# Kernel tuning notes

Hardware: AMD Instinct MI355X
Metric: run time of the kernel (lower is better)

The kernel has to match this reference:

```python
import jax, jax.numpy as jnp
import numpy as np

B, S, H, NH, HD, P, MAXP = 2, 2048, 2048, 16, 128, 2048, 4096
EPS = 1e-06


def setup_inputs() -> dict:
    key = jax.random.key(0)
    ks = jax.random.split(key, 8)
    sc = lambda fan: 1.0 / np.sqrt(fan)
    hidden_states = jax.random.normal(ks[0], (B, S, H), jnp.float32)
    # rotary table: freqs[p] = p * inv_freq, duplicated (non-interleaved) -> [MAXP,1,1,HD]
    inv_freq = 1.0 / (500000.0 ** (np.arange(0, HD, 2, dtype=np.float32) / HD))
    ang = np.outer(np.arange(MAXP, dtype=np.float32), inv_freq)  # [MAXP, HD/2]
    freqs = jnp.asarray(np.concatenate([ang, ang], axis=-1).reshape(MAXP, 1, 1, HD), jnp.float32)
    positions = jnp.tile(jnp.arange(S, dtype=jnp.int32), B)  # [T] = [B*S]
    Wqk = jax.random.normal(ks[1], (2 * P, H), jnp.float32) * sc(H)
    Wv = jax.random.normal(ks[2], (P, H), jnp.float32) * sc(H)
    Wo = jax.random.normal(ks[3], (H, P), jnp.float32) * sc(P)
    conv1_w = jax.random.normal(ks[4], (H // 2, H, 2, 1), jnp.float32) * sc(2 * H)
    conv1_b = jax.random.normal(ks[5], (H // 2,), jnp.float32) * 0.01
    conv2_w = jax.random.normal(ks[6], (H, H // 2, 2, 1), jnp.float32) * sc(H)
    conv2_b = jax.random.normal(ks[7], (H,), jnp.float32) * 0.01
    ln_w = jnp.ones((H,), jnp.float32)
    lf1_cache = jnp.zeros((B, H, 1, 1), jnp.float32)
    lf2_cache = jnp.zeros((B, H // 2, 1, 1), jnp.float32)
    return dict(hidden_states=hidden_states, freqs=freqs, positions=positions,
                Wqk=Wqk, Wv=Wv, Wo=Wo, conv1_w=conv1_w, conv1_b=conv1_b,
                conv2_w=conv2_w, conv2_b=conv2_b, ln_w=ln_w,
                lf1_cache=lf1_cache, lf2_cache=lf2_cache)


def _rmsnorm(x, w, eps=EPS):
    return x * w * jax.lax.rsqrt(jnp.mean(x * x, axis=-1, keepdims=True) + eps)


def _rotate_half(x):
    x1, x2 = jnp.split(x, 2, axis=-1)
    return jnp.concatenate([-x2, x1], axis=-1)


def _forward(hidden_states, freqs, positions, Wqk, Wv, Wo,
             conv1_w, conv1_b, conv2_w, conv2_b, ln_w, lf1_cache, lf2_cache):
    # v projection on raw hidden states
    v = jnp.einsum('bsh,ph->bsp', hidden_states, Wv)  # [B,S,P]

    # --- LocalizedFiltering (causal (2,1) convs with 1-step caches) ---
    x = hidden_states                                     # [B,S,H]
    xc = jnp.concatenate([lf1_cache[:, :, 0, 0][:, None, :], x], axis=1)  # [B,S+1,H]
    w1a, w1b = conv1_w[:, :, 0, 0], conv1_w[:, :, 1, 0]   # [H/2,H]
    y1 = (jnp.einsum('bsh,oh->bso', xc[:, :-1], w1a)
          + jnp.einsum('bsh,oh->bso', xc[:, 1:], w1b) + conv1_b)  # [B,S,H/2]
    y1c = jnp.concatenate([lf2_cache[:, :, 0, 0][:, None, :], y1], axis=1)  # [B,S+1,H/2]
    w2a, w2b = conv2_w[:, :, 0, 0], conv2_w[:, :, 1, 0]   # [H,H/2]
    y2 = (jnp.einsum('bso,ho->bsh', y1c[:, :-1], w2a)
          + jnp.einsum('bso,ho->bsh', y1c[:, 1:], w2b) + conv2_b)  # [B,S,H]
    lf_out = _rmsnorm(y2 + x, ln_w)                       # [B,S,H]
    lf1_new = xc[:, -1][:, :, None, None]                 # [B,H,1,1]
    lf2_new = y1c[:, -1][:, :, None, None]                # [B,H/2,1,1]

    # --- QK projection + RoPE ---
    qk = jnp.einsum('bsh,ph->bsp', lf_out, Wqk).reshape(B, S, NH, 2 * HD)
    q, k = jnp.split(qk, 2, axis=-1)                      # [B,S,NH,HD] each
    f = freqs[positions].reshape(B, S, 1, HD)             # per-token angles
    cos_, sin_ = jnp.cos(f), jnp.sin(f)
    q = q * cos_ + _rotate_half(q) * sin_
    k = k * cos_ + _rotate_half(k) * sin_

    # --- causal SDPA ---
    scale = HD ** -0.5
    vh = v.reshape(B, S, NH, HD)
    scores = jnp.einsum('bqhd,bkhd->bhqk', q, k) * scale  # [B,NH,S,S]
    mask = jnp.tril(jnp.ones((S, S), bool))
    scores = jnp.where(mask, scores, jnp.float32(-1e30))
    probs = jax.nn.softmax(scores, axis=-1)
    attn = jnp.einsum('bhqk,bkhd->bqhd', probs, vh).reshape(B * S, P)

    output = attn @ Wo.T                                  # [T,H]
    return output, lf1_new, lf2_new


def reference(hidden_states, freqs, positions, Wqk, Wv, Wo,
              conv1_w, conv1_b, conv2_w, conv2_b, ln_w, lf1_cache, lf2_cache):
    return _forward(hidden_states, freqs, positions, Wqk, Wv, Wo,
                    conv1_w, conv1_b, conv2_w, conv2_b, ln_w, lf1_cache, lf2_cache)
```

## Files before the change

### kernel.cpp

```cpp
#include <hip/hip_runtime.h>
#include <hip/hip_bf16.h>
#include <stdint.h>

#define Bb 2
#define Ss 2048
#define Hh 2048
#define NHh 16
#define HDd 128
#define Pp 2048
#define Mm 4096

typedef __bf16 bf16x8 __attribute__((ext_vector_type(8)));
typedef float f32x4 __attribute__((ext_vector_type(4)));
typedef float f32x16 __attribute__((ext_vector_type(16)));
typedef __hip_bfloat16 bf16_t;

static __device__ __forceinline__ bf16_t f2b(float f) { return __float2bfloat16(f); }
static __device__ __forceinline__ float b2f(bf16_t b) { return __bfloat162float(b); }

__global__ void k_pack_weights(const float* __restrict__ Wv, const float* __restrict__ Wqk,
                               const float* __restrict__ Wo, const float* __restrict__ c1w,
                               const float* __restrict__ c2w, bf16_t* __restrict__ wv_bf,
                               bf16_t* __restrict__ wqk_bf, bf16_t* __restrict__ wo_bf,
                               bf16_t* __restrict__ w1cat, bf16_t* __restrict__ w2cat) {
  const int M4 = 4 * 1024 * 1024;
  int stride = gridDim.x * blockDim.x;
  for (int i = blockIdx.x * blockDim.x + threadIdx.x; i < 6 * M4; i += stride) {
    if (i < M4) {
      wv_bf[i] = f2b(Wv[i]);
    } else if (i < 3 * M4) {
      int j = i - M4;
      wqk_bf[j] = f2b(Wqk[j]);
    } else if (i < 4 * M4) {
      int j = i - 3 * M4;
      wo_bf[j] = f2b(Wo[j]);
    } else if (i < 5 * M4) {
      int j = i - 4 * M4;
      int o = j >> 12, hp = j & 4095;
      int t = hp >> 11, h = hp & 2047;
      w1cat[j] = f2b(c1w[((size_t)o * 2048 + h) * 2 + t]);
    } else {
      int j = i - 5 * M4;
      int o = j >> 11, cp = j & 2047;
      int t = cp >> 10, c = cp & 1023;
      w2cat[j] = f2b(c2w[((size_t)o * 1024 + c) * 2 + t]);
    }
  }
}

__global__ void k_pack_x(const float* __restrict__ x, const float* __restrict__ lf1,
                         bf16_t* __restrict__ xcat) {
  int stride = gridDim.x * blockDim.x;
  for (int i = blockIdx.x * blockDim.x + threadIdx.x; i < Mm * Hh; i += stride) {
    int m = i >> 11, h = i & 2047;
    int b = m >> 11, s = m & 2047;
    float xv = x[i];
    xcat[(size_t)m * 4096 + 2048 + h] = f2b(xv);
    float xs = (s == 0) ? lf1[b * 2048 + h] : x[i - 2048];
    xcat[(size_t)m * 4096 + h] = f2b(xs);
  }
}

__global__ void k_lf2fill(const float* __restrict__ lf2, bf16_t* __restrict__ y1cat) {
  int i = blockIdx.x * 256 + threadIdx.x;
  if (i >= 2048) return;
  int b = i >> 10, c = i & 1023;
  y1cat[(size_t)(b * 2048) * 2048 + c] = f2b(lf2[b * 1024 + c]);
}

__global__ __launch_bounds__(256) void k_rmsnorm(const float* __restrict__ y2,
                                                 const float* __restrict__ x,
                                                 const float* __restrict__ w,
                                                 bf16_t* __restrict__ out) {
  int m = blockIdx.x;
  const float* yr = y2 + (size_t)m * 2048;
  const float* xr = x + (size_t)m * 2048;
  int tid = threadIdx.x;
  float t[8];
  float ss = 0.0f;
#pragma unroll
  for (int j = 0; j < 8; ++j) {
    int idx = tid + j * 256;
    float v = yr[idx] + xr[idx];
    t[j] = v;
    ss += v * v;
  }
#pragma unroll
  for (int o = 32; o >= 1; o >>= 1) ss += __shfl_xor(ss, o, 64);
  __shared__ float red[4];
  if ((tid & 63) == 0) red[tid >> 6] = ss;
  __syncthreads();
  float tot = red[0] + red[1] + red[2] + red[3];
  float rs = rsqrtf(tot * (1.0f / 2048.0f) + 1e-6f);
#pragma unroll
  for (int j = 0; j < 8; ++j) {
    int idx = tid + j * 256;
    out[(size_t)m * 2048 + idx] = f2b(t[j] * w[idx] * rs);
  }
}

__global__ void k_tails(const float* __restrict__ x, const bf16_t* __restrict__ y1cat,
                        float* __restrict__ out) {
  int i = blockIdx.x * 256 + threadIdx.x;
  if (i >= 4096 + 2048) return;
  const size_t off = (size_t)Mm * Hh;
  if (i < 4096) {
    int b = i >> 11, h = i & 2047;
    out[off + i] = x[((size_t)b * 2048 + 2047) * 2048 + h];
  } else {
    int j = i - 4096;
    int b = j >> 10, c = j & 1023;
    out[off + 4096 + j] = b2f(y1cat[((size_t)b * 2048 + 2047) * 2048 + 1024 + c]);
  }
}

#define EPI_F32 0
#define EPI_Y1CAT 1
#define EPI_ROPE 2
#define EPI_VT 3

template <int EPI, int HAS_BIAS>
__global__ __launch_bounds__(256) void gemm_epi(const bf16_t* __restrict__ A,
                                                const bf16_t* __restrict__ Bw,
                                                void* __restrict__ C1, void* __restrict__ C2,
                                                const float* __restrict__ bias,
                                                const int* __restrict__ posp,
                                                const float* __restrict__ freqs,
                                                int M, int N, int K, int lda) {
  constexpr int SMEM_BYTES = (EPI == EPI_ROPE || EPI == EPI_VT) ? 34816 : 32768;
  __shared__ __align__(16) char smem[SMEM_BYTES];
  bf16_t* lA = (bf16_t*)smem;
  bf16_t* lB = (bf16_t*)(smem + 16384);

  const int tid = threadIdx.x;
  const int lane = tid & 63;
  const int row0 = blockIdx.x * 128;
  const int col0 = blockIdx.y * 128;
  const int wr = ((tid >> 6) >> 1) * 64;
  const int wc = ((tid >> 6) & 1) * 64;
  const int lr = lane & 15;
  const int lg = lane >> 4;

  f32x4 acc[4][4];
#pragma unroll
  for (int i = 0; i < 4; ++i)
#pragma unroll
    for (int j = 0; j < 4; ++j) acc[i][j] = f32x4{0.f, 0.f, 0.f, 0.f};

  for (int k0 = 0; k0 < K; k0 += 64) {
    __syncthreads();
#pragma unroll
    for (int is = 0; is < 4; ++is) {
      const int e = is * 2048 + tid * 8;
      const int r = e >> 6, c = e & 63;
      __builtin_amdgcn_global_load_lds(
          (const __attribute__((address_space(1))) void*)(A + (size_t)(row0 + r) * lda + (k0 + c)),
          (__attribute__((address_space(3))) void*)(&lA[e]), 16, 0, 0);
      __builtin_amdgcn_global_load_lds(
          (const __attribute__((address_space(1))) void*)(Bw + (size_t)(col0 + r) * K + (k0 + c)),
          (__attribute__((address_space(3))) void*)(&lB[e]), 16, 0, 0);
    }
    __syncthreads();
#pragma unroll
    for (int ks = 0; ks < 2; ++ks) {
      bf16x8 af[4], bfg[4];
#pragma unroll
      for (int mi = 0; mi < 4; ++mi)
        af[mi] = *reinterpret_cast<const bf16x8*>(&lA[(wr + mi * 16 + lr) * 64 + ks * 32 + lg * 8]);
#pragma unroll
      for (int ni = 0; ni < 4; ++ni)
        bfg[ni] = *reinterpret_cast<const bf16x8*>(&lB[(wc + ni * 16 + lr) * 64 + ks * 32 + lg * 8]);
#pragma unroll
      for (int mi = 0; mi < 4; ++mi)
#pragma unroll
        for (int ni = 0; ni < 4; ++ni)
          acc[mi][ni] = __builtin_amdgcn_mfma_f32_16x16x32_bf16(af[mi], bfg[ni], acc[mi][ni], 0, 0, 0);
    }
  }

  if constexpr (EPI == EPI_F32) {
#pragma unroll
    for (int mi = 0; mi < 4; ++mi)
#pragma unroll
      for (int ni = 0; ni < 4; ++ni) {
        const int cc = col0 + wc + ni * 16 + lr;
        float bv = HAS_BIAS ? bias[cc] : 0.0f;
#pragma unroll
        for (int r = 0; r < 4; ++r) {
          const int rr = row0 + wr + mi * 16 + lg * 4 + r;
          ((float*)C1)[(size_t)rr * N + cc] = acc[mi][ni][r] + bv;
        }
      }
  } else if constexpr (EPI == EPI_Y1CAT) {
    bf16_t* y1cat = (bf16_t*)C1;
#pragma unroll
    for (int mi = 0; mi < 4; ++mi)
#pragma unroll
      for (int ni = 0; ni < 4; ++ni) {
        const int cc = col0 + wc + ni * 16 + lr;
        float bv = HAS_BIAS ? bias[cc] : 0.0f;
#pragma unroll
        for (int r = 0; r < 4; ++r) {
          const int rr = row0 + wr + mi * 16 + lg * 4 + r;
          bf16_t v = f2b(acc[mi][ni][r] + bv);
          y1cat[(size_t)rr * 2048 + 1024 + cc] = v;
          if ((rr & 2047) != 2047) y1cat[(size_t)(rr + 1) * 2048 + cc] = v;
        }
      }
  } else if constexpr (EPI == EPI_ROPE) {
    __syncthreads();
    bf16_t(*tile)[136] = (bf16_t(*)[136])smem;
#pragma unroll
    for (int mi = 0; mi < 4; ++mi)
#pragma unroll
      for (int ni = 0; ni < 4; ++ni) {
        const int cl = wc + ni * 16 + lr;
#pragma unroll
        for (int r = 0; r < 4; ++r) {
          const int rl = wr + mi * 16 + lg * 4 + r;
          tile[rl][cl] = f2b(acc[mi][ni][r]);
        }
      }
    __syncthreads();
    const int r = tid >> 1, half = tid & 1;
    const int m = row0 + r;
    const int s = m & 2047, bb = m >> 11;
    const int cb = col0 >> 7, h = cb >> 1, isk = cb & 1;
    const int pos = posp[m];
    const float* fr = freqs + (size_t)pos * HDd;
    const float qs = isk ? 1.0f : 0.08838834764831845f;
    bf16_t* dst = (bf16_t*)(isk ? C2 : C1) + ((size_t)(bb * NHh + h) * Ss + s) * HDd + half * 64;
#pragma unroll
    for (int j = 0; j < 8; ++j) {
      bf16x8 lo = *reinterpret_cast<const bf16x8*>(&tile[r][j * 8]);
      bf16x8 hv = *reinterpret_cast<const bf16x8*>(&tile[r][64 + j * 8]);
      bf16x8 ov;
#pragma unroll
      for (int e = 0; e < 8; ++e) {
        float f = fr[j * 8 + e];
        float sn, cs;
        __sincosf(f, &sn, &cs);
        float v0 = b2f((bf16_t)lo[e]), v1 = b2f((bf16_t)hv[e]);
        float o = half ? (v1 * cs + v0 * sn) : (v0 * cs - v1 * sn);
        ov[e] = (__bf16)f2b(o * qs);
      }
      *reinterpret_cast<bf16x8*>(dst + j * 8) = ov;
    }
  } else if constexpr (EPI == EPI_VT) {
    __syncthreads();
    bf16_t(*ttile)[136] = (bf16_t(*)[136])smem;
#pragma unroll
    for (int mi = 0; mi < 4; ++mi)
#pragma unroll
      for (int ni = 0; ni < 4; ++ni) {
        const int cl = wc + ni * 16 + lr;
#pragma unroll
        for (int r = 0; r < 4; ++r) {
          const int rl = wr + mi * 16 + lg * 4 + r;
          ttile[cl][rl] = f2b(acc[mi][ni][r]);
        }
      }
    __syncthreads();
    const int d = tid >> 1, sc = tid & 1;
    const int bb = row0 >> 11, s0 = row0 & 2047, h = col0 >> 7;
    bf16_t* dst = (bf16_t*)C1 + ((size_t)(bb * NHh + h) * HDd + d) * Ss + s0 + sc * 64;
#pragma unroll
    for (int j = 0; j < 8; ++j)
      *reinterpret_cast<bf16x8*>(dst + j * 8) =
          *reinterpret_cast<const bf16x8*>(&ttile[d][sc * 64 + j * 8]);
  }
}

__global__ __launch_bounds__(256) void k_attn3(const bf16_t* __restrict__ qa,
                                               const bf16_t* __restrict__ ka,
                                               const bf16_t* __restrict__ vt,
                                               bf16_t* __restrict__ attn_out) {
  __shared__ bf16_t kbuf[64 * 128];
  __shared__ bf16_t vbuf[128 * 64];
  __shared__ bf16_t pbuf[4][32 * 64];

  const int tid = threadIdx.x;
  const int wave = tid >> 6, lane = tid & 63;
  const int l31 = lane & 31, hi = lane >> 5;
  const int bh = blockIdx.x;
  const int yy = blockIdx.y;
  const int jq = (yy < 8) ? (15 - yy) : (yy - 8);
  const int q0b = jq * 128;
  const int q0w = q0b + wave * 32;
  const int b = bh >> 4, h = bh & 15;

  const bf16_t* Q = qa + (size_t)bh * Ss * HDd;
  const bf16_t* K = ka + (size_t)bh * Ss * HDd;
  const bf16_t* V = vt + (size_t)bh * HDd * Ss;
  char* pw = (char*)&pbuf[wave][0];

  bf16x8 qf[8];
#pragma unroll
  for (int dc = 0; dc < 8; ++dc)
    qf[dc] = *reinterpret_cast<const bf16x8*>(&Q[(size_t)(q0w + l31) * HDd + dc * 16 + hi * 8]);

  f32x16 o[4];
#pragma unroll
  for (int db = 0; db < 4; ++db)
#pragma unroll
    for (int i = 0; i < 16; ++i) o[db][i] = 0.f;
  float mrun = -3e38f, lrun = 0.f;
  const int qrow = q0w + l31;

  const int nkt = q0b / 64 + 2;
  bf16x8 pk[4], pv[4];
  auto loadt = [&](int kt) {
    const int k0l = kt * 64;
#pragma unroll
    for (int i = 0; i < 4; ++i) {
      pk[i] = *reinterpret_cast<const bf16x8*>(
          &K[(size_t)(k0l + (tid >> 2)) * HDd + ((tid & 3) + 4 * i) * 8]);
      pv[i] = *reinterpret_cast<const bf16x8*>(
          &V[(size_t)(tid >> 1) * Ss + k0l + ((tid & 1) * 4 + i) * 8]);
    }
  };
  loadt(0);

  for (int kt = 0; kt < nkt; ++kt) {
    const int k0 = kt * 64;
    __syncthreads();
    {
      const int kr = tid >> 2, vr = tid >> 1;
#pragma unroll
      for (int i = 0; i < 4; ++i) {
        const int ku = (tid & 3) + 4 * i;
        *reinterpret_cast<bf16x8*>((char*)kbuf + kr * 256 + ((ku * 16) ^ ((kr & 7) << 4))) = pk[i];
        const int vu = (tid & 1) * 4 + i;
        *reinterpret_cast<bf16x8*>((char*)vbuf + vr * 128 + ((vu * 16) ^ ((vr & 7) << 4))) = pv[i];
      }
    }
    __syncthreads();
    if (kt + 1 < nkt) loadt(kt + 1);
    if (k0 > q0w + 31) continue;

    f32x16 s0, s1;
#pragma unroll
    for (int i = 0; i < 16; ++i) { s0[i] = 0.f; s1[i] = 0.f; }
    __builtin_amdgcn_s_setprio(1);
#pragma unroll
    for (int dc = 0; dc < 8; ++dc) {
      const int off = (dc * 32 + hi * 16) ^ ((l31 & 7) << 4);
      bf16x8 kf0 = *reinterpret_cast<const bf16x8*>((const char*)kbuf + l31 * 256 + off);
      bf16x8 kf1 = *reinterpret_cast<const bf16x8*>((const char*)kbuf + (32 + l31) * 256 + off);
      s0 = __builtin_amdgcn_mfma_f32_32x32x16_bf16(kf0, qf[dc], s0, 0, 0, 0);
      s1 = __builtin_amdgcn_mfma_f32_32x32x16_bf16(kf1, qf[dc], s1, 0, 0, 0);
    }
    __builtin_amdgcn_s_setprio(0);
    if (k0 + 63 > q0w) {
#pragma unroll
      for (int reg = 0; reg < 16; ++reg) {
        const int key = k0 + (reg & 3) + 8 * (reg >> 2) + 4 * hi;
        if (key > qrow) s0[reg] = -1e30f;
        if (key + 32 > qrow) s1[reg] = -1e30f;
      }
    }
    float pm = fmaxf(s0[0], s1[0]);
#pragma unroll
    for (int reg = 1; reg < 16; ++reg) pm = fmaxf(pm, fmaxf(s0[reg], s1[reg]));
    pm = fmaxf(pm, __shfl_xor(pm, 32, 64));
    if (!__all(pm - mrun <= 8.0f)) {
      const float mnew = fmaxf(mrun, pm);
      const float alpha = __expf(mrun - mnew);
      lrun *= alpha;
#pragma unroll
      for (int reg = 0; reg < 16; ++reg) {
        const int r = (reg & 3) + 8 * (reg >> 2) + 4 * hi;
        const float ar = __shfl(alpha, r, 64);
        o[0][reg] *= ar; o[1][reg] *= ar; o[2][reg] *= ar; o[3][reg] *= ar;
      }
      mrun = mnew;
    }
    float psum = 0.f;
#pragma unroll
    for (int reg = 0; reg < 16; ++reg) {
      s0[reg] = __expf(s0[reg] - mrun); psum += s0[reg];
      s1[reg] = __expf(s1[reg] - mrun); psum += s1[reg];
    }
    psum += __shfl_xor(psum, 32, 64);
    lrun += psum;
#pragma unroll
    for (int g = 0; g < 4; ++g) {
      uint32_t w0, w1, w2, w3;
      asm("v_cvt_pk_bf16_f32 %0, %1, %2" : "=v"(w0) : "v"(s0[4 * g]), "v"(s0[4 * g + 1]));
      asm("v_cvt_pk_bf16_f32 %0, %1, %2" : "=v"(w1) : "v"(s0[4 * g + 2]), "v"(s0[4 * g + 3]));
      asm("v_cvt_pk_bf16_f32 %0, %1, %2" : "=v"(w2) : "v"(s1[4 * g]), "v"(s1[4 * g + 1]));
      asm("v_cvt_pk_bf16_f32 %0, %1, %2" : "=v"(w3) : "v"(s1[4 * g + 2]), "v"(s1[4 * g + 3]));
      const int key0 = 8 * g + 4 * hi;
      const int sw = (l31 & 7) << 4;
      *reinterpret_cast<uint2*>(pw + l31 * 128 + ((key0 * 2) ^ sw)) = uint2{w0, w1};
      *reinterpret_cast<uint2*>(pw + l31 * 128 + (((key0 + 32) * 2) ^ sw)) = uint2{w2, w3};
    }
    __builtin_amdgcn_s_setprio(1);
#pragma unroll
    for (int kc = 0; kc < 4; ++kc) {
      bf16x8 pa = *reinterpret_cast<const bf16x8*>(
          pw + l31 * 128 + ((kc * 32 + hi * 16) ^ ((l31 & 7) << 4)));
#pragma unroll
      for (int db = 0; db < 4; ++db) {
        const int d = db * 32 + l31;
        bf16x8 vf = *reinterpret_cast<const bf16x8*>(
            (const char*)vbuf + d * 128 + ((kc * 32 + hi * 16) ^ ((d & 7) << 4)));
        o[db] = __builtin_amdgcn_mfma_f32_32x32x16_bf16(pa, vf, o[db], 0, 0, 0);
      }
    }
    __builtin_amdgcn_s_setprio(0);
  }
  const float linv = 1.0f / lrun;
#pragma unroll
  for (int reg = 0; reg < 16; ++reg) {
    const int r = (reg & 3) + 8 * (reg >> 2) + 4 * hi;
    const float li = __shfl(linv, r, 64);
    const int qr = q0w + r;
#pragma unroll
    for (int db = 0; db < 4; ++db) {
      attn_out[(size_t)(b * 2048 + qr) * 2048 + h * 128 + db * 32 + l31] = f2b(o[db][reg] * li);
    }
  }
}

extern "C" void kernel_launch(void* const* d_in, const int* in_sizes, int n_in,
                              void* d_out, int out_size, void* d_ws, size_t ws_size,
                              hipStream_t stream) {
  const float* x     = (const float*)d_in[0];
  const float* freqs = (const float*)d_in[1];
  const int*   pos   = (const int*)d_in[2];
  const float* Wqk   = (const float*)d_in[3];
  const float* Wv    = (const float*)d_in[4];
  const float* Wo    = (const float*)d_in[5];
  const float* c1w   = (const float*)d_in[6];
  const float* c1b   = (const float*)d_in[7];
  const float* c2w   = (const float*)d_in[8];
  const float* c2b   = (const float*)d_in[9];
  const float* lnw   = (const float*)d_in[10];
  const float* lf1   = (const float*)d_in[11];
  const float* lf2   = (const float*)d_in[12];
  float* out = (float*)d_out;

  char* ws = (char*)d_ws;
  const size_t MB = 1024 * 1024;
  bf16_t* wv_bf  = (bf16_t*)(ws + 0 * MB);
  bf16_t* w1cat  = (bf16_t*)(ws + 8 * MB);
  bf16_t* wqk_bf = (bf16_t*)(ws + 16 * MB);
  bf16_t* wo_bf  = (bf16_t*)(ws + 32 * MB);
  bf16_t* w2cat  = (bf16_t*)(ws + 40 * MB);
  bf16_t* xcat   = (bf16_t*)(ws + 48 * MB);
  bf16_t* y1cat  = (bf16_t*)(ws + 80 * MB);
  bf16_t* vt_att = (bf16_t*)(ws + 96 * MB);
  bf16_t* q_att  = (bf16_t*)(ws + 112 * MB);
  float*  y2_f   = (float*)(ws + 48 * MB);
  bf16_t* lfo_bf = (bf16_t*)(ws + 80 * MB);
  bf16_t* k_att  = (bf16_t*)(ws + 0 * MB);
  bf16_t* attn_b = (bf16_t*)(ws + 48 * MB);

  k_pack_weights<<<2048, 256, 0, stream>>>(Wv, Wqk, Wo, c1w, c2w, wv_bf, wqk_bf, wo_bf,
                                           w1cat, w2cat);
  k_pack_x<<<2048, 256, 0, stream>>>(x, lf1, xcat);
  k_lf2fill<<<8, 256, 0, stream>>>(lf2, y1cat);

  gemm_epi<EPI_VT, 0><<<dim3(Mm / 128, 2048 / 128), 256, 0, stream>>>(
      xcat + 2048, wv_bf, vt_att, nullptr, nullptr, nullptr, nullptr, Mm, 2048, 2048, 4096);
  gemm_epi<EPI_Y1CAT, 1><<<dim3(Mm / 128, 1024 / 128), 256, 0, stream>>>(
      xcat, w1cat, y1cat, nullptr, c1b, nullptr, nullptr, Mm, 1024, 4096, 4096);
  k_tails<<<24, 256, 0, stream>>>(x, y1cat, out);
  gemm_epi<EPI_F32, 1><<<dim3(Mm / 128, 2048 / 128), 256, 0, stream>>>(
      y1cat, w2cat, y2_f, nullptr, c2b, nullptr, nullptr, Mm, 2048, 2048, 2048);
  k_rmsnorm<<<Mm, 256, 0, stream>>>(y2_f, x, lnw, lfo_bf);
  gemm_epi<EPI_ROPE, 0><<<dim3(Mm / 128, 4096 / 128), 256, 0, stream>>>(
      lfo_bf, wqk_bf, q_att, k_att, nullptr, pos, freqs, Mm, 4096, 2048, 2048);
  k_attn3<<<dim3(Bb * NHh, Ss / 128), 256, 0, stream>>>(q_att, k_att, vt_att, attn_b);
  gemm_epi<EPI_F32, 0><<<dim3(Mm / 128, 2048 / 128), 256, 0, stream>>>(
      attn_b, wo_bf, out, nullptr, nullptr, nullptr, nullptr, Mm, 2048, 2048, 2048);
}
```

Measured before the change: 644.5 us.

## Double-buffer GEMM LDS tiles and vectorize pack and RMSNorm kernels

The GEMM main loop now uses two 32 KB LDS buffers, issuing the async global-to-LDS loads for the next K tile before computing on the current one, with one barrier per iteration and raised wave priority around the MFMA block. This is meant to hide global-load latency behind matrix math. The x-packing and RMSNorm kernels switch to float4 loads and packed bf16 stores to cut memory instructions. LDS per block grows to 64 KB, which can lower occupancy. The epilogue scratch that previously sat past 32 KB must still fit in the enlarged buffer.

```diff
diff --git a/kernel.cpp b/kernel.cpp
--- a/kernel.cpp
+++ b/kernel.cpp
@@ -51,13 +51,21 @@
 __global__ void k_pack_x(const float* __restrict__ x, const float* __restrict__ lf1,
                          bf16_t* __restrict__ xcat) {
   int stride = gridDim.x * blockDim.x;
-  for (int i = blockIdx.x * blockDim.x + threadIdx.x; i < Mm * Hh; i += stride) {
-    int m = i >> 11, h = i & 2047;
+  const int n4 = Mm * Hh / 4;
+  for (int i = blockIdx.x * blockDim.x + threadIdx.x; i < n4; i += stride) {
+    int e = i * 4;
+    int m = e >> 11, h = e & 2047;
     int b = m >> 11, s = m & 2047;
-    float xv = x[i];
-    xcat[(size_t)m * 4096 + 2048 + h] = f2b(xv);
-    float xs = (s == 0) ? lf1[b * 2048 + h] : x[i - 2048];
-    xcat[(size_t)m * 4096 + h] = f2b(xs);
+    float4 xv = *reinterpret_cast<const float4*>(&x[e]);
+    bf16_t o4[4];
+    o4[0] = f2b(xv.x); o4[1] = f2b(xv.y); o4[2] = f2b(xv.z); o4[3] = f2b(xv.w);
+    *reinterpret_cast<uint64_t*>(&xcat[(size_t)m * 4096 + 2048 + h]) =
+        *reinterpret_cast<const uint64_t*>(o4);
+    float4 xs = (s == 0) ? *reinterpret_cast<const float4*>(&lf1[b * 2048 + h])
+                         : *reinterpret_cast<const float4*>(&x[e - 2048]);
+    o4[0] = f2b(xs.x); o4[1] = f2b(xs.y); o4[2] = f2b(xs.z); o4[3] = f2b(xs.w);
+    *reinterpret_cast<uint64_t*>(&xcat[(size_t)m * 4096 + h]) =
+        *reinterpret_cast<const uint64_t*>(o4);
   }
 }
 
@@ -76,15 +84,16 @@
   const float* yr = y2 + (size_t)m * 2048;
   const float* xr = x + (size_t)m * 2048;
   int tid = threadIdx.x;
-  float t[8];
+  const int base = tid * 8;
+  float4 ya = *reinterpret_cast<const float4*>(yr + base);
+  float4 yb = *reinterpret_cast<const float4*>(yr + base + 4);
+  float4 xa = *reinterpret_cast<const float4*>(xr + base);
+  float4 xb = *reinterpret_cast<const float4*>(xr + base + 4);
+  float t[8] = {ya.x + xa.x, ya.y + xa.y, ya.z + xa.z, ya.w + xa.w,
+                yb.x + xb.x, yb.y + xb.y, yb.z + xb.z, yb.w + xb.w};
   float ss = 0.0f;
 #pragma unroll
-  for (int j = 0; j < 8; ++j) {
-    int idx = tid + j * 256;
-    float v = yr[idx] + xr[idx];
-    t[j] = v;
-    ss += v * v;
-  }
+  for (int j = 0; j < 8; ++j) ss += t[j] * t[j];
 #pragma unroll
   for (int o = 32; o >= 1; o >>= 1) ss += __shfl_xor(ss, o, 64);
   __shared__ float red[4];
@@ -92,11 +101,14 @@
   __syncthreads();
   float tot = red[0] + red[1] + red[2] + red[3];
   float rs = rsqrtf(tot * (1.0f / 2048.0f) + 1e-6f);
-#pragma unroll
-  for (int j = 0; j < 8; ++j) {
-    int idx = tid + j * 256;
-    out[(size_t)m * 2048 + idx] = f2b(t[j] * w[idx] * rs);
-  }
+  float4 wa = *reinterpret_cast<const float4*>(w + base);
+  float4 wb = *reinterpret_cast<const float4*>(w + base + 4);
+  float wv[8] = {wa.x, wa.y, wa.z, wa.w, wb.x, wb.y, wb.z, wb.w};
+  bf16_t o8[8];
+#pragma unroll
+  for (int j = 0; j < 8; ++j) o8[j] = f2b(t[j] * wv[j] * rs);
+  *reinterpret_cast<uint4*>(&out[(size_t)m * 2048 + base]) =
+      *reinterpret_cast<const uint4*>(o8);
 }
 
 __global__ void k_tails(const float* __restrict__ x, const bf16_t* __restrict__ y1cat,
@@ -127,10 +139,7 @@
                                                 const int* __restrict__ posp,
                                                 const float* __restrict__ freqs,
                                                 int M, int N, int K, int lda) {
-  constexpr int SMEM_BYTES = (EPI == EPI_ROPE || EPI == EPI_VT) ? 34816 : 32768;
-  __shared__ __align__(16) char smem[SMEM_BYTES];
-  bf16_t* lA = (bf16_t*)smem;
-  bf16_t* lB = (bf16_t*)(smem + 16384);
+  __shared__ __align__(16) char smem[65536];
 
   const int tid = threadIdx.x;
   const int lane = tid & 63;
@@ -147,35 +156,49 @@
 #pragma unroll
     for (int j = 0; j < 4; ++j) acc[i][j] = f32x4{0.f, 0.f, 0.f, 0.f};
 
-  for (int k0 = 0; k0 < K; k0 += 64) {
-    __syncthreads();
+  auto stage = [&](int buf, int k0) {
+    bf16_t* dA = (bf16_t*)(smem + buf * 32768);
+    bf16_t* dB = (bf16_t*)(smem + buf * 32768 + 16384);
 #pragma unroll
     for (int is = 0; is < 4; ++is) {
       const int e = is * 2048 + tid * 8;
       const int r = e >> 6, c = e & 63;
       __builtin_amdgcn_global_load_lds(
           (const __attribute__((address_space(1))) void*)(A + (size_t)(row0 + r) * lda + (k0 + c)),
-          (__attribute__((address_space(3))) void*)(&lA[e]), 16, 0, 0);
+          (__attribute__((address_space(3))) void*)(&dA[e]), 16, 0, 0);
       __builtin_amdgcn_global_load_lds(
           (const __attribute__((address_space(1))) void*)(Bw + (size_t)(col0 + r) * K + (k0 + c)),
-          (__attribute__((address_space(3))) void*)(&lB[e]), 16, 0, 0);
-    }
-    __syncthreads();
+          (__attribute__((address_space(3))) void*)(&dB[e]), 16, 0, 0);
+    }
+  };
+
+  const int nt = K / 64;
+  stage(0, 0);
+  __syncthreads();
+  for (int t = 0; t < nt; ++t) {
+    const int cur = t & 1;
+    if (t + 1 < nt) stage(cur ^ 1, (t + 1) * 64);
+    __builtin_amdgcn_sched_barrier(0);
+    const bf16_t* sA = (const bf16_t*)(smem + cur * 32768);
+    const bf16_t* sB = (const bf16_t*)(smem + cur * 32768 + 16384);
+    __builtin_amdgcn_s_setprio(1);
 #pragma unroll
     for (int ks = 0; ks < 2; ++ks) {
       bf16x8 af[4], bfg[4];
 #pragma unroll
       for (int mi = 0; mi < 4; ++mi)
-        af[mi] = *reinterpret_cast<const bf16x8*>(&lA[(wr + mi * 16 + lr) * 64 + ks * 32 + lg * 8]);
+        af[mi] = *reinterpret_cast<const bf16x8*>(&sA[(wr + mi * 16 + lr) * 64 + ks * 32 + lg * 8]);
 #pragma unroll
       for (int ni = 0; ni < 4; ++ni)
-        bfg[ni] = *reinterpret_cast<const bf16x8*>(&lB[(wc + ni * 16 + lr) * 64 + ks * 32 + lg * 8]);
+        bfg[ni] = *reinterpret_cast<const bf16x8*>(&sB[(wc + ni * 16 + lr) * 64 + ks * 32 + lg * 8]);
 #pragma unroll
       for (int mi = 0; mi < 4; ++mi)
 #pragma unroll
         for (int ni = 0; ni < 4; ++ni)
           acc[mi][ni] = __builtin_amdgcn_mfma_f32_16x16x32_bf16(af[mi], bfg[ni], acc[mi][ni], 0, 0, 0);
     }
+    __builtin_amdgcn_s_setprio(0);
+    __syncthreads();
   }
 
   if constexpr (EPI == EPI_F32) {
```

Result: faster. 580.4 us (-9.9%).
